# Kernel tuning notes

Hardware: AMD Instinct MI355X
Metric: run time of the kernel (lower is better)

The kernel has to match this reference:

```python
import jax, jax.numpy as jnp
import numpy as np


def setup_inputs() -> dict:
    key = jax.random.key(0)
    k1, k2 = jax.random.split(key)
    N, M, D = 16384, 16384, 3
    src_V = jax.random.normal(k1, (N, D), dtype=jnp.float32)
    tar_V = jax.random.normal(k2, (M, D), dtype=jnp.float32)
    return {"src_V": src_V, "tar_V": tar_V}


def reference(src_V, tar_V):
    # 1-NN: for each target point find nearest source point (replaces cKDTree).
    # Squared distances via ||t||^2 - 2 t.s + ||s||^2 ; [M, N]
    d2 = (
        jnp.sum(tar_V * tar_V, axis=1, keepdims=True)
        - 2.0 * (tar_V @ src_V.T)
        + jnp.sum(src_V * src_V, axis=1)[None, :]
    )
    ii = jnp.argmin(d2, axis=1)            # [M] nearest src index per target
    diff = src_V[ii] - tar_V               # [M, 3]
    loss = 0.5 * jnp.sum(diff * diff)
    return loss
```

## Files before the change

kernel.cpp:

```cpp
#include <hip/hip_runtime.h>
#include <math.h>

constexpr int N_SRC = 16384;
constexpr int M_TAR = 16384;

constexpr int BLOCKS = 512;
constexpr int TPB = 512;
constexpr int CHUNKS = 256;
constexpr int TPT = 16;
constexpr int NROWS = N_SRC / CHUNKS;

__global__ void prep(const float* __restrict__ src,
                     float4* __restrict__ ws,
                     float* __restrict__ out) {
    int i = blockIdx.x * blockDim.x + threadIdx.x;
    if (i == 0) out[0] = 0.0f;
    const float* q = src + 3 * i;
    float x = q[0], y = q[1], z = q[2];
    ws[i] = make_float4(x, y, z, fmaf(x, x, fmaf(y, y, z * z)));
}

__device__ __forceinline__ void min3(float& b, float e0, float e1) {
    asm("v_min3_f32 %0, %0, %1, %2"
        : "+v"(b) : "v"(e0), "v"(e1));
}

__device__ __forceinline__ float to_sgpr(float x) {
    return __uint_as_float(
        (unsigned)__builtin_amdgcn_readfirstlane((int)__float_as_uint(x)));
}

__global__ __launch_bounds__(TPB, 2)
void nn14(const float4* __restrict__ ws,
          const float* __restrict__ src,
          const float* __restrict__ tar,
          float* __restrict__ out) {
    __shared__ float fv[32 * CHUNKS];

    const int tid   = threadIdx.x;
    const int g     = tid >> 8;
    const int chunk = tid & 255;
    const int tbase = blockIdx.x * 32;

    float txm2[TPT], tym2[TPT], tzm2[TPT], best[TPT];
#pragma unroll
    for (int k = 0; k < TPT; ++k) {
        int T = tbase + g * TPT + k;
        txm2[k] = to_sgpr(-2.0f * tar[3 * T + 0]);
        tym2[k] = to_sgpr(-2.0f * tar[3 * T + 1]);
        tzm2[k] = to_sgpr(-2.0f * tar[3 * T + 2]);
        best[k] = INFINITY;
    }

    auto comp = [&](float4 s0, float4 s1) {
#pragma unroll
        for (int k = 0; k < TPT; ++k) {
            float t0 = fmaf(s0.z, tzm2[k], s0.w);
            t0 = fmaf(s0.y, tym2[k], t0);
            t0 = fmaf(s0.x, txm2[k], t0);
            float t1 = fmaf(s1.z, tzm2[k], s1.w);
            t1 = fmaf(s1.y, tym2[k], t1);
            t1 = fmaf(s1.x, txm2[k], t1);
            min3(best[k], t0, t1);
        }
    };

    float4 s0 = ws[0 * CHUNKS + chunk];
    float4 s1 = ws[1 * CHUNKS + chunk];
#pragma unroll 1
    for (int r = 0; r + 2 < NROWS; r += 2) {
        float4 n0 = ws[(r + 2) * CHUNKS + chunk];
        float4 n1 = ws[(r + 3) * CHUNKS + chunk];
        __builtin_amdgcn_sched_barrier(0);
        comp(s0, s1);
        s0 = n0; s1 = n1;
    }
    comp(s0, s1);

#pragma unroll
    for (int k = 0; k < TPT; ++k) {
        fv[(g * TPT + k) * CHUNKS + chunk] = best[k];
    }
    __syncthreads();

    const int tprime = tid >> 4;
    const int sub    = tid & 15;
    float bv = fv[tprime * CHUNKS + sub];
    int   bc = sub;
#pragma unroll
    for (int m = 1; m < CHUNKS / 16; ++m) {
        float v = fv[tprime * CHUNKS + sub + 16 * m];
        if (v < bv) { bv = v; bc = sub + 16 * m; }
    }
#pragma unroll
    for (int s = 8; s >= 1; s >>= 1) {
        float vv = __shfl_xor(bv, s, 64);
        int   cc = __shfl_xor(bc, s, 64);
        if (vv < bv) { bv = vv; bc = cc; }
    }

    const int T = tbase + tprime;
    const float tx = tar[3 * T + 0], ty = tar[3 * T + 1], tz = tar[3 * T + 2];
    const float rxm2 = -2.0f * tx, rym2 = -2.0f * ty, rzm2 = -2.0f * tz;
    int myrow = NROWS;
#pragma unroll
    for (int rr = 0; rr < NROWS / 16; ++rr) {
        int r = sub + 16 * rr;
        int j = r * CHUNKS + bc;
        const float* q = src + 3 * j;
        float x = q[0], y = q[1], z = q[2];
        float w = fmaf(x, x, fmaf(y, y, z * z));
        float v = fmaf(z, rzm2, w);
        v = fmaf(y, rym2, v);
        v = fmaf(x, rxm2, v);
        if (v == bv && r < myrow) myrow = r;
    }
#pragma unroll
    for (int s = 8; s >= 1; s >>= 1) {
        int r2 = __shfl_xor(myrow, s, 64);
        if (r2 < myrow) myrow = r2;
    }
    __syncthreads();

    if (sub == 0) {
        int j = myrow * CHUNKS + bc;
        float dx = src[3 * j + 0] - tx;
        float dy = src[3 * j + 1] - ty;
        float dz = src[3 * j + 2] - tz;
        fv[tprime] = 0.5f * fmaf(dx, dx, fmaf(dy, dy, dz * dz));
    }
    __syncthreads();
    if (tid == 0) {
        float ssum = 0.0f;
#pragma unroll
        for (int i = 0; i < 32; ++i) ssum += fv[i];
        atomicAdd(out, ssum);
    }
}

extern "C" void kernel_launch(void* const* d_in, const int* in_sizes, int n_in,
                              void* d_out, int out_size, void* d_ws, size_t ws_size,
                              hipStream_t stream) {
    const float* src = (const float*)d_in[0];
    const float* tar = (const float*)d_in[1];
    float* out = (float*)d_out;
    float4* ws = (float4*)d_ws;
    (void)ws_size;

    prep<<<N_SRC / 512, 512, 0, stream>>>(src, ws, out);
    nn14<<<BLOCKS, TPB, 0, stream>>>(ws, src, tar, out);
}
```

Measured before the change: 85.07 us.

## Widen blocks to 1024 threads, fold -2 scaling into source norms, deepen prefetch

Doubles threads per block and source chunks to 512, so each block covers all sources with half as many rows per thread. Rescales the distance metric to -0.5*||s||^2 + t·s and maximizes it. This lets target coordinates be used directly, loaded from a wave-uniform pointer rather than read and moved to SGPRs one by one. Adds a two-stage prefetch with unroll 2 and simplifies the row-recovery step to one candidate per lane. The risks are higher register pressure and LDS use at 1024 threads, and tie-break behaviour that depends on exactly reproducing the floating-point value.

```diff
diff --git a/kernel.cpp b/kernel.cpp
--- a/kernel.cpp
+++ b/kernel.cpp
@@ -5,8 +5,8 @@
 constexpr int M_TAR = 16384;
 
 constexpr int BLOCKS = 512;
-constexpr int TPB = 512;
-constexpr int CHUNKS = 256;
+constexpr int TPB = 1024;
+constexpr int CHUNKS = 512;
 constexpr int TPT = 16;
 constexpr int NROWS = N_SRC / CHUNKS;
 
@@ -17,65 +17,64 @@
     if (i == 0) out[0] = 0.0f;
     const float* q = src + 3 * i;
     float x = q[0], y = q[1], z = q[2];
-    ws[i] = make_float4(x, y, z, fmaf(x, x, fmaf(y, y, z * z)));
+    ws[i] = make_float4(x, y, z, -0.5f * fmaf(x, x, fmaf(y, y, z * z)));
 }
 
-__device__ __forceinline__ void min3(float& b, float e0, float e1) {
-    asm("v_min3_f32 %0, %0, %1, %2"
+__device__ __forceinline__ void max3(float& b, float e0, float e1) {
+    asm("v_max3_f32 %0, %0, %1, %2"
         : "+v"(b) : "v"(e0), "v"(e1));
 }
 
-__device__ __forceinline__ float to_sgpr(float x) {
-    return __uint_as_float(
-        (unsigned)__builtin_amdgcn_readfirstlane((int)__float_as_uint(x)));
-}
-
 __global__ __launch_bounds__(TPB, 2)
-void nn14(const float4* __restrict__ ws,
+void nn15(const float4* __restrict__ ws,
           const float* __restrict__ src,
           const float* __restrict__ tar,
           float* __restrict__ out) {
     __shared__ float fv[32 * CHUNKS];
 
     const int tid   = threadIdx.x;
-    const int g     = tid >> 8;
-    const int chunk = tid & 255;
+    const int g     = tid >> 9;
+    const int chunk = tid & 511;
     const int tbase = blockIdx.x * 32;
 
-    float txm2[TPT], tym2[TPT], tzm2[TPT], best[TPT];
+    const int gu = __builtin_amdgcn_readfirstlane(g);
+    const float* tw = tar + 3 * (tbase + gu * TPT);
+    float tx[TPT], ty[TPT], tz[TPT], best[TPT];
 #pragma unroll
     for (int k = 0; k < TPT; ++k) {
-        int T = tbase + g * TPT + k;
-        txm2[k] = to_sgpr(-2.0f * tar[3 * T + 0]);
-        tym2[k] = to_sgpr(-2.0f * tar[3 * T + 1]);
-        tzm2[k] = to_sgpr(-2.0f * tar[3 * T + 2]);
-        best[k] = INFINITY;
+        tx[k] = tw[3 * k + 0];
+        ty[k] = tw[3 * k + 1];
+        tz[k] = tw[3 * k + 2];
+        best[k] = -INFINITY;
     }
 
     auto comp = [&](float4 s0, float4 s1) {
 #pragma unroll
         for (int k = 0; k < TPT; ++k) {
-            float t0 = fmaf(s0.z, tzm2[k], s0.w);
-            t0 = fmaf(s0.y, tym2[k], t0);
-            t0 = fmaf(s0.x, txm2[k], t0);
-            float t1 = fmaf(s1.z, tzm2[k], s1.w);
-            t1 = fmaf(s1.y, tym2[k], t1);
-            t1 = fmaf(s1.x, txm2[k], t1);
-            min3(best[k], t0, t1);
+            float t0 = fmaf(s0.z, tz[k], s0.w);
+            t0 = fmaf(s0.y, ty[k], t0);
+            t0 = fmaf(s0.x, tx[k], t0);
+            float t1 = fmaf(s1.z, tz[k], s1.w);
+            t1 = fmaf(s1.y, ty[k], t1);
+            t1 = fmaf(s1.x, tx[k], t1);
+            max3(best[k], t0, t1);
         }
     };
 
     float4 s0 = ws[0 * CHUNKS + chunk];
     float4 s1 = ws[1 * CHUNKS + chunk];
-#pragma unroll 1
-    for (int r = 0; r + 2 < NROWS; r += 2) {
-        float4 n0 = ws[(r + 2) * CHUNKS + chunk];
-        float4 n1 = ws[(r + 3) * CHUNKS + chunk];
+    float4 n0 = ws[2 * CHUNKS + chunk];
+    float4 n1 = ws[3 * CHUNKS + chunk];
+#pragma unroll 2
+    for (int r = 0; r + 4 < NROWS; r += 2) {
+        float4 f0 = ws[(r + 4) * CHUNKS + chunk];
+        float4 f1 = ws[(r + 5) * CHUNKS + chunk];
         __builtin_amdgcn_sched_barrier(0);
         comp(s0, s1);
-        s0 = n0; s1 = n1;
+        s0 = n0; s1 = n1; n0 = f0; n1 = f1;
     }
     comp(s0, s1);
+    comp(n0, n1);
 
 #pragma unroll
     for (int k = 0; k < TPT; ++k) {
@@ -83,40 +82,37 @@
     }
     __syncthreads();
 
-    const int tprime = tid >> 4;
-    const int sub    = tid & 15;
+    const int tprime = tid >> 5;
+    const int sub    = tid & 31;
     float bv = fv[tprime * CHUNKS + sub];
     int   bc = sub;
 #pragma unroll
-    for (int m = 1; m < CHUNKS / 16; ++m) {
-        float v = fv[tprime * CHUNKS + sub + 16 * m];
-        if (v < bv) { bv = v; bc = sub + 16 * m; }
+    for (int m = 1; m < CHUNKS / 32; ++m) {
+        float v = fv[tprime * CHUNKS + sub + 32 * m];
+        if (v > bv) { bv = v; bc = sub + 32 * m; }
     }
 #pragma unroll
-    for (int s = 8; s >= 1; s >>= 1) {
+    for (int s = 16; s >= 1; s >>= 1) {
         float vv = __shfl_xor(bv, s, 64);
         int   cc = __shfl_xor(bc, s, 64);
-        if (vv < bv) { bv = vv; bc = cc; }
+        if (vv > bv) { bv = vv; bc = cc; }
     }
 
     const int T = tbase + tprime;
-    const float tx = tar[3 * T + 0], ty = tar[3 * T + 1], tz = tar[3 * T + 2];
-    const float rxm2 = -2.0f * tx, rym2 = -2.0f * ty, rzm2 = -2.0f * tz;
-    int myrow = NROWS;
-#pragma unroll
-    for (int rr = 0; rr < NROWS / 16; ++rr) {
-        int r = sub + 16 * rr;
-        int j = r * CHUNKS + bc;
+    const float qx = tar[3 * T + 0], qy = tar[3 * T + 1], qz = tar[3 * T + 2];
+    int myrow;
+    {
+        int j = sub * CHUNKS + bc;
         const float* q = src + 3 * j;
         float x = q[0], y = q[1], z = q[2];
-        float w = fmaf(x, x, fmaf(y, y, z * z));
-        float v = fmaf(z, rzm2, w);
-        v = fmaf(y, rym2, v);
-        v = fmaf(x, rxm2, v);
-        if (v == bv && r < myrow) myrow = r;
+        float h = -0.5f * fmaf(x, x, fmaf(y, y, z * z));
+        float v = fmaf(z, qz, h);
+        v = fmaf(y, qy, v);
+        v = fmaf(x, qx, v);
+        myrow = (v == bv) ? sub : NROWS;
     }
 #pragma unroll
-    for (int s = 8; s >= 1; s >>= 1) {
+    for (int s = 16; s >= 1; s >>= 1) {
         int r2 = __shfl_xor(myrow, s, 64);
         if (r2 < myrow) myrow = r2;
     }
@@ -124,9 +120,9 @@
 
     if (sub == 0) {
         int j = myrow * CHUNKS + bc;
-        float dx = src[3 * j + 0] - tx;
-        float dy = src[3 * j + 1] - ty;
-        float dz = src[3 * j + 2] - tz;
+        float dx = src[3 * j + 0] - qx;
+        float dy = src[3 * j + 1] - qy;
+        float dz = src[3 * j + 2] - qz;
         fv[tprime] = 0.5f * fmaf(dx, dx, fmaf(dy, dy, dz * dz));
     }
     __syncthreads();
@@ -148,5 +144,5 @@
     (void)ws_size;
 
     prep<<<N_SRC / 512, 512, 0, stream>>>(src, ws, out);
-    nn14<<<BLOCKS, TPB, 0, stream>>>(ws, src, tar, out);
+    nn15<<<BLOCKS, TPB, 0, stream>>>(ws, src, tar, out);
 }
```

New measurement: 87.29 us. 2.6% more time.
